# Kernel tuning notes

Hardware: AMD Instinct MI355X
Metric: run time of the kernel (lower is better)

## Reference

```python
import jax, jax.numpy as jnp
import numpy as np

B, V, C, H, W = 2, 4, 64, 256, 256
RADIUS = 2.0
R = 2  # integer splat footprint half-width = ceil(RADIUS)
EPS = 1e-8
FOCAL = 256.0


def _rt(tx, ty, tz):
    M = np.eye(4, dtype=np.float32)
    M[0, 3], M[1, 3], M[2, 3] = tx, ty, tz
    return M


def setup_inputs() -> dict:
    key = jax.random.key(0)
    k1, k2 = jax.random.split(key)
    feats = jax.random.normal(k1, (B, V, C, H, W), dtype=jnp.float32)
    # depths in [1, 5): positive, realistic metric range
    depths = 1.0 + 4.0 * jax.random.uniform(k2, (B, V, 1, H, W), dtype=jnp.float32)
    Km = np.eye(4, dtype=np.float32)
    Km[0, 0] = FOCAL; Km[1, 1] = FOCAL
    Km[0, 2] = W / 2.0; Km[1, 2] = H / 2.0
    K = jnp.asarray(np.tile(Km[None], (B, 1, 1)))
    src = np.stack([_rt(0.05 * v, 0.0, 0.0) for v in range(V)], 0)  # (V,4,4)
    src_RTs = jnp.asarray(np.tile(src[None], (B, 1, 1, 1)))
    src_RTinvs = jnp.linalg.inv(src_RTs)
    dst = _rt(0.02, 0.0, 0.1)
    dst_RTs = jnp.asarray(np.tile(dst[None, None], (B, 1, 1, 1)))
    dst_RTinvs = jnp.linalg.inv(dst_RTs)
    return {"feats": feats, "depths": depths, "K": K, "src_RTs": src_RTs,
            "src_RTinvs": src_RTinvs, "dst_RTs": dst_RTs, "dst_RTinvs": dst_RTinvs}


def _project_and_splat(feats, depths, K, src_RTinvs, dst_RTs):
    Bn, Vn, Cn, Hn, Wn = feats.shape
    N = Hn * Wn
    BV = Bn * Vn
    # pixel grid (homogeneous image coords), row-major so flat idx = y*W + x
    xs = jnp.arange(Wn, dtype=feats.dtype)
    ys = jnp.arange(Hn, dtype=feats.dtype)
    gx, gy = jnp.meshgrid(xs, ys, indexing="xy")  # (H,W)
    gx = gx.reshape(-1); gy = gy.reshape(-1)      # (N,)
    d = depths.reshape(Bn, Vn, 1, N)
    ones = jnp.ones_like(d)
    # view_to_world_coord: [x*d, y*d, d, 1] -> K^-1 -> RTinv
    proj = jnp.concatenate([gx * d, gy * d, d, ones], axis=2)  # (B,V,4,N)
    Kinv = jnp.linalg.inv(K)
    cam = jnp.einsum("bij,bvjn->bvin", Kinv, proj)
    world = jnp.einsum("bvij,bvjn->bvin", src_RTinvs, cam)
    # world_to_view: dst RT -> K -> perspective divide
    cam2 = jnp.einsum("bij,bvjn->bvin", dst_RTs.reshape(Bn, 4, 4), world)
    xyp = jnp.einsum("bij,bvjn->bvin", K, cam2)
    z = xyp[:, :, 2].reshape(BV, N)
    x = (xyp[:, :, 0] / (xyp[:, :, 2] + EPS)).reshape(BV, N)
    y = (xyp[:, :, 1] / (xyp[:, :, 2] + EPS)).reshape(BV, N)
    # radius splatting: scatter-accumulate over a (2R+1)^2 footprint,
    # linear falloff in pixel distance, soft z-buffer via 1/z weighting
    fN = feats.reshape(BV, Cn, N).transpose(0, 2, 1)  # (BV,N,C)
    acc = jnp.zeros((BV * N, Cn), feats.dtype)
    wz = jnp.zeros((BV * N, 2), feats.dtype)  # [:,0]=sum w, [:,1]=sum w*z
    boff = (jnp.arange(BV) * N)[:, None]
    px0 = jnp.round(x); py0 = jnp.round(y)
    invz = 1.0 / (z + EPS)
    for dy in range(-R, R + 1):
        for dx in range(-R, R + 1):
            px = px0 + dx; py = py0 + dy
            dist = jnp.sqrt((px - x) ** 2 + (py - y) ** 2 + EPS)
            w = jnp.maximum(0.0, 1.0 - dist / RADIUS)
            valid = (px >= 0) & (px < Wn) & (py >= 0) & (py < Hn) & (z > EPS)
            w = jnp.where(valid, w * invz, 0.0)
            ix = jnp.clip(px.astype(jnp.int32), 0, Wn - 1)
            iy = jnp.clip(py.astype(jnp.int32), 0, Hn - 1)
            idx = (boff + iy * Wn + ix).reshape(-1)
            acc = acc.at[idx].add((w[..., None] * fN).reshape(-1, Cn))
            wz = wz.at[idx].add(jnp.stack([w, w * z], -1).reshape(-1, 2))
    wsum = wz[:, 0:1]; zsum = wz[:, 1:2]
    prj_feats = (acc / (wsum + EPS)).reshape(Bn, Vn, Hn, Wn, Cn).transpose(0, 1, 4, 2, 3)
    prj_depth = (zsum / (wsum + EPS)).reshape(Bn, Vn, Hn, Wn, 1).transpose(0, 1, 4, 2, 3)
    return jnp.concatenate([prj_feats, prj_depth], axis=2)  # (B,V,C+1,H,W)


def reference(feats, depths, K, src_RTs, src_RTinvs, dst_RTs, dst_RTinvs):
    return _project_and_splat(feats, depths, K, src_RTinvs, dst_RTs)
```

## Files before the change

### kernel.cpp

```cpp
#include <hip/hip_runtime.h>

#define Wd 256
#define Hd 256
#define Nn 65536
#define Cc 64
#define Vv 4
#define Bb 2
#define BVn 8
#define NREC ((size_t)BVn * Nn)
#define EPSf 1e-8f

#define OFF_COUNT   ((size_t)0)
#define OFF_OFFS    ((size_t)2  << 20)
#define OFF_CURS    ((size_t)4  << 20)
#define OFF_ROWSUM  ((size_t)6  << 20)
#define OFF_ROWBASE (((size_t)6 << 20) + 65536)
#define OFF_STAGE1  ((size_t)8  << 20)
#define OFF_BINNED  ((size_t)16 << 20)
#define OFF_FT      ((size_t)24 << 20)
#define FT_BYTES    ((size_t)BVn * Nn * Cc * 4)
#define NEED_FULL   (OFF_FT + FT_BYTES)
#define NEED_MID    OFF_FT

__device__ inline void mat4_mul(const float* A, const float* B, float* C) {
#pragma unroll
  for (int i = 0; i < 4; i++)
#pragma unroll
    for (int j = 0; j < 4; j++) {
      float s = 0.f;
#pragma unroll
      for (int k = 0; k < 4; k++) s += A[i * 4 + k] * B[k * 4 + j];
      C[i * 4 + j] = s;
    }
}

__device__ inline void mat4_inv(const float* m, float* invOut) {
  float inv[16];
  inv[0] = m[5]*m[10]*m[15] - m[5]*m[11]*m[14] - m[9]*m[6]*m[15] +
           m[9]*m[7]*m[14] + m[13]*m[6]*m[11] - m[13]*m[7]*m[10];
  inv[4] = -m[4]*m[10]*m[15] + m[4]*m[11]*m[14] + m[8]*m[6]*m[15] -
           m[8]*m[7]*m[14] - m[12]*m[6]*m[11] + m[12]*m[7]*m[10];
  inv[8] = m[4]*m[9]*m[15] - m[4]*m[11]*m[13] - m[8]*m[5]*m[15] +
           m[8]*m[7]*m[13] + m[12]*m[5]*m[11] - m[12]*m[7]*m[9];
  inv[12] = -m[4]*m[9]*m[14] + m[4]*m[10]*m[13] + m[8]*m[5]*m[14] -
            m[8]*m[6]*m[13] - m[12]*m[5]*m[10] + m[12]*m[6]*m[9];
  inv[1] = -m[1]*m[10]*m[15] + m[1]*m[11]*m[14] + m[9]*m[2]*m[15] -
           m[9]*m[3]*m[14] - m[13]*m[2]*m[11] + m[13]*m[3]*m[10];
  inv[5] = m[0]*m[10]*m[15] - m[0]*m[11]*m[14] - m[8]*m[2]*m[15] +
           m[8]*m[3]*m[14] + m[12]*m[2]*m[11] - m[12]*m[3]*m[10];
  inv[9] = -m[0]*m[9]*m[15] + m[0]*m[11]*m[13] + m[8]*m[1]*m[15] -
           m[8]*m[3]*m[13] - m[12]*m[1]*m[11] + m[12]*m[3]*m[9];
  inv[13] = m[0]*m[9]*m[14] - m[0]*m[10]*m[13] - m[8]*m[1]*m[14] +
            m[8]*m[2]*m[13] + m[12]*m[1]*m[10] - m[12]*m[2]*m[9];
  inv[2] = m[1]*m[6]*m[15] - m[1]*m[7]*m[14] - m[5]*m[2]*m[15] +
           m[5]*m[3]*m[14] + m[13]*m[2]*m[7] - m[13]*m[3]*m[6];
  inv[6] = -m[0]*m[6]*m[15] + m[0]*m[7]*m[14] + m[4]*m[2]*m[15] -
           m[4]*m[3]*m[14] - m[12]*m[2]*m[7] + m[12]*m[3]*m[6];
  inv[10] = m[0]*m[5]*m[15] - m[0]*m[7]*m[13] - m[4]*m[1]*m[15] +
            m[4]*m[3]*m[13] + m[12]*m[1]*m[7] - m[12]*m[3]*m[5];
  inv[14] = -m[0]*m[5]*m[14] + m[0]*m[6]*m[13] + m[4]*m[1]*m[14] -
            m[4]*m[2]*m[13] - m[12]*m[1]*m[6] + m[12]*m[2]*m[5];
  inv[3] = -m[1]*m[6]*m[11] + m[1]*m[7]*m[10] + m[5]*m[2]*m[11] -
           m[5]*m[3]*m[10] - m[9]*m[2]*m[7] + m[9]*m[3]*m[6];
  inv[7] = m[0]*m[6]*m[11] - m[0]*m[7]*m[10] - m[4]*m[2]*m[11] +
           m[4]*m[3]*m[10] + m[8]*m[2]*m[7] - m[8]*m[3]*m[6];
  inv[11] = -m[0]*m[5]*m[11] + m[0]*m[7]*m[9] + m[4]*m[1]*m[11] -
            m[4]*m[3]*m[9] - m[8]*m[1]*m[7] + m[8]*m[3]*m[5];
  inv[15] = m[0]*m[5]*m[10] - m[0]*m[6]*m[9] - m[4]*m[1]*m[10] +
            m[4]*m[2]*m[9] + m[8]*m[1]*m[6] - m[8]*m[2]*m[5];
  float det = m[0]*inv[0] + m[1]*inv[4] + m[2]*inv[8] + m[3]*inv[12];
  det = 1.0f / det;
#pragma unroll
  for (int i = 0; i < 16; i++) invOut[i] = inv[i] * det;
}

__device__ inline void compute_T(const float* Kmat, const float* srcinv,
                                 const float* dstRT, int b, int bv, float* T) {
  float Kinv[16], M1[16], M2[16];
  mat4_inv(Kmat + b * 16, Kinv);
  mat4_mul(srcinv + bv * 16, Kinv, M1);
  mat4_mul(dstRT + b * 16, M1, M2);
  mat4_mul(Kmat + b * 16, M2, T);
}

__global__ __launch_bounds__(256) void project_count_kernel(
    const float* __restrict__ depths, const float* __restrict__ Kmat,
    const float* __restrict__ srcinv, const float* __restrict__ dstRT,
    unsigned int* __restrict__ counts, float4* __restrict__ stage1) {
  const int bv = blockIdx.x >> 8;
  const int n = ((blockIdx.x & 255) << 8) | threadIdx.x;
  const int b = bv >> 2;

  __shared__ float T[16];
  if (threadIdx.x == 0) compute_T(Kmat, srcinv, dstRT, b, bv, T);
  __syncthreads();

  const float d = depths[(size_t)bv * Nn + n];
  const float gx = (float)(n & (Wd - 1));
  const float gy = (float)(n >> 8);

  const float p0 = (T[0] * gx + T[1] * gy + T[2]) * d + T[3];
  const float p1 = (T[4] * gx + T[5] * gy + T[6]) * d + T[7];
  const float z  = (T[8] * gx + T[9] * gy + T[10]) * d + T[11];

  const float ze = z + EPSf;
  const float x = p0 / ze;
  const float y = p1 / ze;
  const float px0 = rintf(x);
  const float py0 = rintf(y);

  int bin = -1;
  if (z > EPSf && px0 >= -2.0f && px0 <= (float)(Wd + 1) &&
      py0 >= -2.0f && py0 <= (float)(Hd + 1)) {
    const int bx = min(max((int)px0, 0), Wd - 1);
    const int by = min(max((int)py0, 0), Hd - 1);
    bin = (bv << 16) | (by << 8) | bx;
    atomicAdd(&counts[bin], 1u);
  }
  float4 rec;
  rec.x = x; rec.y = y; rec.z = z; rec.w = __int_as_float(bin);
  stage1[(size_t)bv * Nn + n] = rec;
}

__global__ __launch_bounds__(256) void row_sum_kernel(
    const unsigned int* __restrict__ counts, unsigned int* __restrict__ rowsum) {
  const int wid = threadIdx.x >> 6;
  const int lane = threadIdx.x & 63;
  const int r = blockIdx.x * 4 + wid;
  const uint4 c = reinterpret_cast<const uint4*>(counts + (size_t)r * 256)[lane];
  unsigned int s = c.x + c.y + c.z + c.w;
#pragma unroll
  for (int off = 32; off > 0; off >>= 1) s += __shfl_down(s, off, 64);
  if (lane == 0) rowsum[r] = s;
}

__global__ __launch_bounds__(256) void scan_rows_kernel(
    const unsigned int* __restrict__ rowsum, unsigned int* __restrict__ rowbase) {
  __shared__ unsigned int part[256];
  const int t = threadIdx.x;
  unsigned int loc[8];
  unsigned int run = 0;
#pragma unroll
  for (int i = 0; i < 8; i++) {
    loc[i] = run;
    run += rowsum[t * 8 + i];
  }
  part[t] = run;
  __syncthreads();
  for (int off = 1; off < 256; off <<= 1) {
    unsigned int x = part[t];
    unsigned int y = (t >= off) ? part[t - off] : 0u;
    __syncthreads();
    part[t] = x + y;
    __syncthreads();
  }
  const unsigned int base = (t == 0) ? 0u : part[t - 1];
#pragma unroll
  for (int i = 0; i < 8; i++) rowbase[t * 8 + i] = base + loc[i];
}

__global__ __launch_bounds__(256) void bin_offsets_kernel(
    const unsigned int* __restrict__ counts, const unsigned int* __restrict__ rowbase,
    unsigned int* __restrict__ offs, unsigned int* __restrict__ curs) {
  const int wid = threadIdx.x >> 6;
  const int lane = threadIdx.x & 63;
  const int r = blockIdx.x * 4 + wid;
  const uint4 c = reinterpret_cast<const uint4*>(counts + (size_t)r * 256)[lane];
  const unsigned int t0 = c.x;
  const unsigned int t1 = t0 + c.y;
  const unsigned int t2 = t1 + c.z;
  const unsigned int t3 = t2 + c.w;
  unsigned int inc = t3;
#pragma unroll
  for (int off = 1; off < 64; off <<= 1) {
    const unsigned int v = __shfl_up(inc, off, 64);
    if (lane >= off) inc += v;
  }
  const unsigned int base = rowbase[r] + inc - t3;
  uint4 o;
  o.x = base;
  o.y = base + t0;
  o.z = base + t1;
  o.w = base + t2;
  reinterpret_cast<uint4*>(offs + (size_t)r * 256)[lane] = o;
  reinterpret_cast<uint4*>(curs + (size_t)r * 256)[lane] = o;
}

template <bool FSTAGED>
__global__ __launch_bounds__(256) void fill_kernel(
    const float* __restrict__ feats, const float4* __restrict__ stage1,
    unsigned int* __restrict__ curs, float4* __restrict__ binned,
    float4* __restrict__ binnedF) {
  const int g = blockIdx.x * 256 + threadIdx.x;
  float4 rec = stage1[g];
  const int bin = __float_as_int(rec.w);
  if (bin >= 0) {
    const unsigned int slot = atomicAdd(&curs[bin], 1u);
    const int n = g & (Nn - 1);
    if (FSTAGED) {
      rec.w = 1.0f / (rec.z + EPSf);
      binned[slot] = rec;
      const int bv = g >> 16;
      const float* fp = feats + ((size_t)bv * Cc << 16) + n;
#pragma unroll
      for (int cgi = 0; cgi < 4; cgi++) {
        float4* dst = binnedF + (((size_t)cgi * NREC + slot) << 2);
#pragma unroll
        for (int i = 0; i < 4; i++) {
          const int c0 = cgi * 16 + 4 * i;
          float4 v;
          v.x = fp[(size_t)(c0 + 0) << 16];
          v.y = fp[(size_t)(c0 + 1) << 16];
          v.z = fp[(size_t)(c0 + 2) << 16];
          v.w = fp[(size_t)(c0 + 3) << 16];
          dst[i] = v;
        }
      }
    } else {
      rec.w = __int_as_float(n);
      binned[slot] = rec;
    }
  }
}

template <bool FSTAGED>
__global__ __launch_bounds__(256) void gather_kernel(
    const float* __restrict__ feats,
    const unsigned int* __restrict__ offs, const unsigned int* __restrict__ curs,
    const float4* __restrict__ binned, const float4* __restrict__ binnedF,
    float* __restrict__ out) {
  const int cpx = gridDim.x >> 3;
  const int orig = (blockIdx.x & 7) * cpx + (blockIdx.x >> 3);
  const int bv = orig >> 10;
  const int cg = (orig >> 8) & 3;
  const int vrow = orig & 255;
  const int u = threadIdx.x;

  float acc[16];
#pragma unroll
  for (int c = 0; c < 16; c++) acc[c] = 0.f;
  float wsum = 0.f, wz = 0.f;

  const float uf = (float)u, vf = (float)vrow;
  const int by_lo = max(0, vrow - 2), by_hi = min(Hd - 1, vrow + 2);
  const int bx_lo = max(0, u - 2), bx_hi = min(Wd - 1, u + 2);

  const float4* plane = binnedF + (((size_t)cg * NREC) << 2);

  for (int by = by_lo; by <= by_hi; by++) {
    const int rowb = (bv << 16) | (by << 8);
    const unsigned int s = offs[rowb + bx_lo];
    const unsigned int e = curs[rowb + bx_hi];
    if (FSTAGED) {
      if (s >= e) continue;
      float4 rec = binned[s];
      const float4* fs0 = plane + ((size_t)s << 2);
      float4 f0 = fs0[0], f1 = fs0[1], f2 = fs0[2], f3 = fs0[3];
      for (unsigned int r = s; r < e; r++) {
        const unsigned int rn = (r + 1 < e) ? r + 1 : r;
        const float4 rec_n = binned[rn];
        const float4* fsn = plane + ((size_t)rn << 2);
        const float4 g0 = fsn[0], g1 = fsn[1], g2 = fsn[2], g3 = fsn[3];

        const float ddx = uf - rec.x;
        const float ddy = vf - rec.y;
        const float dist = sqrtf(ddx * ddx + ddy * ddy + EPSf);
        const float w = fmaxf(0.0f, 1.0f - dist * 0.5f) * rec.w;
        wsum += w;
        wz += w * rec.z;
        acc[0]  += w * f0.x; acc[1]  += w * f0.y;
        acc[2]  += w * f0.z; acc[3]  += w * f0.w;
        acc[4]  += w * f1.x; acc[5]  += w * f1.y;
        acc[6]  += w * f1.z; acc[7]  += w * f1.w;
        acc[8]  += w * f2.x; acc[9]  += w * f2.y;
        acc[10] += w * f2.z; acc[11] += w * f2.w;
        acc[12] += w * f3.x; acc[13] += w * f3.y;
        acc[14] += w * f3.z; acc[15] += w * f3.w;

        rec = rec_n;
        f0 = g0; f1 = g1; f2 = g2; f3 = g3;
      }
    } else {
      for (unsigned int r = s; r < e; r++) {
        const float4 rec = binned[r];
        const float ddx = uf - rec.x;
        const float ddy = vf - rec.y;
        const float dist = sqrtf(ddx * ddx + ddy * ddy + EPSf);
        float w = 1.0f - dist * 0.5f;
        if (w > 0.f) {
          w *= 1.0f / (rec.z + EPSf);
          wsum += w;
          wz += w * rec.z;
          const int n = __float_as_int(rec.w);
          const float* fp = feats + ((size_t)bv * Cc << 16) + n;
#pragma unroll
          for (int c = 0; c < 16; c++)
            acc[c] += w * fp[(size_t)(cg * 16 + c) << 16];
        }
      }
    }
  }

  const float inv = 1.0f / (wsum + EPSf);
  const int dest = (vrow << 8) | u;
  float* ob = out + (((size_t)bv * 65) << 16) + ((size_t)(cg * 16) << 16) + dest;
#pragma unroll
  for (int c = 0; c < 16; c++) ob[(size_t)c << 16] = acc[c] * inv;
  if (cg == 0) {
    out[(((size_t)bv * 65 + Cc) << 16) + dest] = wz * inv;
  }
}

__global__ __launch_bounds__(256) void splat_kernel(
    const float* __restrict__ feats, const float* __restrict__ depths,
    const float* __restrict__ Kmat, const float* __restrict__ srcinv,
    const float* __restrict__ dstRT, float* __restrict__ out,
    float* __restrict__ wsum) {
  const int bv = blockIdx.x >> 8;
  const int n = ((blockIdx.x & 255) << 8) | threadIdx.x;
  const int b = bv >> 2;

  __shared__ float T[16];
  if (threadIdx.x == 0) compute_T(Kmat, srcinv, dstRT, b, bv, T);
  __syncthreads();

  const float d = depths[(size_t)bv * Nn + n];
  const float gx = (float)(n & (Wd - 1));
  const float gy = (float)(n >> 8);
  const float p0 = (T[0] * gx + T[1] * gy + T[2]) * d + T[3];
  const float p1 = (T[4] * gx + T[5] * gy + T[6]) * d + T[7];
  const float z  = (T[8] * gx + T[9] * gy + T[10]) * d + T[11];
  const float ze = z + EPSf;
  const float x = p0 / ze, y = p1 / ze;
  const float zi = 1.0f / ze;
  const float px0 = rintf(x), py0 = rintf(y);
  const bool zok = (z > EPSf);

  float f[Cc];
  const float* fp = feats + (size_t)bv * Cc * Nn + n;
#pragma unroll
  for (int c = 0; c < Cc; c++) f[c] = fp[(size_t)c * Nn];

  float* outbv = out + (size_t)bv * 65 * Nn;
  float* wbv = wsum + (size_t)bv * Nn;
#pragma unroll
  for (int dy = -2; dy <= 2; dy++) {
#pragma unroll
    for (int dx = -2; dx <= 2; dx++) {
      const float px = px0 + (float)dx;
      const float py = py0 + (float)dy;
      const float ddx = px - x, ddy = py - y;
      const float dist = sqrtf(ddx * ddx + ddy * ddy + EPSf);
      float w = fmaxf(0.0f, 1.0f - dist * 0.5f);
      const bool valid = zok && (px >= 0.0f) && (px < (float)Wd) &&
                         (py >= 0.0f) && (py < (float)Hd);
      w = valid ? w * zi : 0.0f;
      if (w > 0.0f) {
        const int idx = (int)py * Wd + (int)px;
        atomicAdd(wbv + idx, w);
        atomicAdd(outbv + (size_t)Cc * Nn + idx, w * z);
#pragma unroll
        for (int c = 0; c < Cc; c++)
          atomicAdd(outbv + (size_t)c * Nn + idx, w * f[c]);
      }
    }
  }
}

__global__ __launch_bounds__(256) void norm_kernel(float* __restrict__ out,
                                                   const float* __restrict__ wsum) {
  const int t = blockIdx.x * 256 + threadIdx.x;
  const int n = t & 0xFFFF;
  const int bvc = t >> 16;
  const int bv = bvc / 65;
  const float wv = wsum[(size_t)bv * Nn + n];
  out[t] = out[t] / (wv + EPSf);
}

extern "C" void kernel_launch(void* const* d_in, const int* in_sizes, int n_in,
                              void* d_out, int out_size, void* d_ws, size_t ws_size,
                              hipStream_t stream) {
  const float* feats  = (const float*)d_in[0];
  const float* depths = (const float*)d_in[1];
  const float* Kmat   = (const float*)d_in[2];
  const float* srcinv = (const float*)d_in[4];
  const float* dstRT  = (const float*)d_in[5];
  float* out = (float*)d_out;
  char* ws = (char*)d_ws;

  if (ws_size >= NEED_MID) {
    unsigned int* counts = (unsigned int*)(ws + OFF_COUNT);
    unsigned int* offs   = (unsigned int*)(ws + OFF_OFFS);
    unsigned int* curs   = (unsigned int*)(ws + OFF_CURS);
    unsigned int* rowsum = (unsigned int*)(ws + OFF_ROWSUM);
    unsigned int* rowbase= (unsigned int*)(ws + OFF_ROWBASE);
    float4* stage1 = (float4*)(ws + OFF_STAGE1);
    float4* binned = (float4*)(ws + OFF_BINNED);
    float4* binnedF= (float4*)(ws + OFF_FT);

    hipMemsetAsync(counts, 0, (size_t)BVn * Nn * sizeof(unsigned int), stream);

    const bool staged = (ws_size >= NEED_FULL);

    project_count_kernel<<<dim3(BVn * (Nn / 256)), dim3(256), 0, stream>>>(
        depths, Kmat, srcinv, dstRT, counts, stage1);
    row_sum_kernel<<<dim3(512), dim3(256), 0, stream>>>(counts, rowsum);
    scan_rows_kernel<<<dim3(1), dim3(256), 0, stream>>>(rowsum, rowbase);
    bin_offsets_kernel<<<dim3(512), dim3(256), 0, stream>>>(counts, rowbase, offs, curs);

    if (staged) {
      fill_kernel<true><<<dim3(BVn * Nn / 256), dim3(256), 0, stream>>>(
          feats, stage1, curs, binned, binnedF);
      gather_kernel<true><<<dim3(BVn * 4 * Hd), dim3(256), 0, stream>>>(
          feats, offs, curs, binned, binnedF, out);
    } else {
      fill_kernel<false><<<dim3(BVn * Nn / 256), dim3(256), 0, stream>>>(
          feats, stage1, curs, binned, binnedF);
      gather_kernel<false><<<dim3(BVn * 4 * Hd), dim3(256), 0, stream>>>(
          feats, offs, curs, binned, binnedF, out);
    }
  } else {
    float* wsum = (float*)ws;
    hipMemsetAsync(out, 0, (size_t)out_size * sizeof(float), stream);
    hipMemsetAsync(wsum, 0, (size_t)BVn * Nn * sizeof(float), stream);
    splat_kernel<<<dim3(BVn * (Nn / 256)), dim3(256), 0, stream>>>(
        feats, depths, Kmat, srcinv, dstRT, out, wsum);
    norm_kernel<<<dim3(BVn * 65 * Nn / 256), dim3(256), 0, stream>>>(out, wsum);
  }
}
```

Before: 705.1 us.

## Split gather channels across four threads per pixel to raise parallelism

The gather kernel now gives each output pixel's 16-channel group to four threads, each holding four accumulators and loading one float4 of staged features per record. The grid grows fourfold, with each block covering a quarter-row segment. The goal is fewer registers, more occupancy and shorter per-thread loops. In exchange, the record-header and distance/weight work is repeated across the four threads, the manual prefetch is dropped, and output stores are less coalesced because only 64 pixels share each block.

```diff
diff --git a/kernel.cpp b/kernel.cpp
--- a/kernel.cpp
+++ b/kernel.cpp
@@ -231,14 +231,17 @@
     float* __restrict__ out) {
   const int cpx = gridDim.x >> 3;
   const int orig = (blockIdx.x & 7) * cpx + (blockIdx.x >> 3);
-  const int bv = orig >> 10;
-  const int cg = (orig >> 8) & 3;
-  const int vrow = orig & 255;
-  const int u = threadIdx.x;
-
-  float acc[16];
-#pragma unroll
-  for (int c = 0; c < 16; c++) acc[c] = 0.f;
+  const int bv = orig >> 12;
+  const int cg = (orig >> 10) & 3;
+  const int vrow = (orig >> 2) & 255;
+  const int seg = orig & 3;
+  const int g = threadIdx.x >> 2;
+  const int k = threadIdx.x & 3;
+  const int u = (seg << 6) | g;
+
+  float acc[4];
+#pragma unroll
+  for (int c = 0; c < 4; c++) acc[c] = 0.f;
   float wsum = 0.f, wz = 0.f;
 
   const float uf = (float)u, vf = (float)vrow;
@@ -252,33 +255,19 @@
     const unsigned int s = offs[rowb + bx_lo];
     const unsigned int e = curs[rowb + bx_hi];
     if (FSTAGED) {
-      if (s >= e) continue;
-      float4 rec = binned[s];
-      const float4* fs0 = plane + ((size_t)s << 2);
-      float4 f0 = fs0[0], f1 = fs0[1], f2 = fs0[2], f3 = fs0[3];
       for (unsigned int r = s; r < e; r++) {
-        const unsigned int rn = (r + 1 < e) ? r + 1 : r;
-        const float4 rec_n = binned[rn];
-        const float4* fsn = plane + ((size_t)rn << 2);
-        const float4 g0 = fsn[0], g1 = fsn[1], g2 = fsn[2], g3 = fsn[3];
-
+        const float4 rec = binned[r];
+        const float4 f = plane[((size_t)r << 2) + k];
         const float ddx = uf - rec.x;
         const float ddy = vf - rec.y;
         const float dist = sqrtf(ddx * ddx + ddy * ddy + EPSf);
         const float w = fmaxf(0.0f, 1.0f - dist * 0.5f) * rec.w;
         wsum += w;
         wz += w * rec.z;
-        acc[0]  += w * f0.x; acc[1]  += w * f0.y;
-        acc[2]  += w * f0.z; acc[3]  += w * f0.w;
-        acc[4]  += w * f1.x; acc[5]  += w * f1.y;
-        acc[6]  += w * f1.z; acc[7]  += w * f1.w;
-        acc[8]  += w * f2.x; acc[9]  += w * f2.y;
-        acc[10] += w * f2.z; acc[11] += w * f2.w;
-        acc[12] += w * f3.x; acc[13] += w * f3.y;
-        acc[14] += w * f3.z; acc[15] += w * f3.w;
-
-        rec = rec_n;
-        f0 = g0; f1 = g1; f2 = g2; f3 = g3;
+        acc[0] += w * f.x;
+        acc[1] += w * f.y;
+        acc[2] += w * f.z;
+        acc[3] += w * f.w;
       }
     } else {
       for (unsigned int r = s; r < e; r++) {
@@ -294,8 +283,8 @@
           const int n = __float_as_int(rec.w);
           const float* fp = feats + ((size_t)bv * Cc << 16) + n;
 #pragma unroll
-          for (int c = 0; c < 16; c++)
-            acc[c] += w * fp[(size_t)(cg * 16 + c) << 16];
+          for (int c = 0; c < 4; c++)
+            acc[c] += w * fp[(size_t)(cg * 16 + k * 4 + c) << 16];
         }
       }
     }
@@ -303,10 +292,11 @@
 
   const float inv = 1.0f / (wsum + EPSf);
   const int dest = (vrow << 8) | u;
-  float* ob = out + (((size_t)bv * 65) << 16) + ((size_t)(cg * 16) << 16) + dest;
-#pragma unroll
-  for (int c = 0; c < 16; c++) ob[(size_t)c << 16] = acc[c] * inv;
-  if (cg == 0) {
+  float* ob = out + (((size_t)bv * 65) << 16) +
+              ((size_t)(cg * 16 + k * 4) << 16) + dest;
+#pragma unroll
+  for (int c = 0; c < 4; c++) ob[(size_t)c << 16] = acc[c] * inv;
+  if (cg == 0 && k == 0) {
     out[(((size_t)bv * 65 + Cc) << 16) + dest] = wz * inv;
   }
 }
@@ -411,12 +401,12 @@
     if (staged) {
       fill_kernel<true><<<dim3(BVn * Nn / 256), dim3(256), 0, stream>>>(
           feats, stage1, curs, binned, binnedF);
-      gather_kernel<true><<<dim3(BVn * 4 * Hd), dim3(256), 0, stream>>>(
+      gather_kernel<true><<<dim3(BVn * 4 * Hd * 4), dim3(256), 0, stream>>>(
           feats, offs, curs, binned, binnedF, out);
     } else {
       fill_kernel<false><<<dim3(BVn * Nn / 256), dim3(256), 0, stream>>>(
           feats, stage1, curs, binned, binnedF);
-      gather_kernel<false><<<dim3(BVn * 4 * Hd), dim3(256), 0, stream>>>(
+      gather_kernel<false><<<dim3(BVn * 4 * Hd * 4), dim3(256), 0, stream>>>(
           feats, offs, curs, binned, binnedF, out);
     }
   } else {
```

Result: faster. 648.5 us (-8.0%).
